# Kernel tuning notes

Hardware: AMD Instinct MI355X
Metric: run time of the kernel (lower is better)

## Reference

```python
import jax, jax.numpy as jnp
import numpy as np

WINDOW_SIZE = 100  # band half-width = WINDOW_SIZE // 2 = 50, inclusive


def setup_inputs() -> dict:
    key = jax.random.key(0)
    kq, kk, kv = jax.random.split(key, 3)
    shape = (2, 8, 4096, 64)  # [B, H, S, D]
    return {
        "query": jax.random.normal(kq, shape, dtype=jnp.float32),
        "key": jax.random.normal(kk, shape, dtype=jnp.float32),
        "value": jax.random.normal(kv, shape, dtype=jnp.float32),
    }


def reference(query, key, value):
    B, H, S, D = query.shape
    half = WINDOW_SIZE // 2
    scale = 1.0 / jnp.sqrt(jnp.asarray(D, dtype=jnp.float32))
    # Full dense scores (faithful to the original module): [B, H, S, S]
    scores = jnp.einsum("bhqd,bhkd->bhqk", query, key) * scale
    # Sliding-window band mask: row i attends to j in [i-half, i+half]
    idx = jnp.arange(S)
    band = jnp.abs(idx[:, None] - idx[None, :]) <= half  # [S, S]
    scores = jnp.where(band[None, None, :, :], scores, -jnp.inf)
    attn = jax.nn.softmax(scores, axis=-1)
    attn = jnp.nan_to_num(attn, nan=0.0)  # matches torch.nan_to_num(w, 0.0)
    return jnp.einsum("bhqk,bhkd->bhqd", attn, value)
```

## Files before the change

### kernel.cpp

```cpp
#include <hip/hip_runtime.h>

#define S_LEN 4096
#define DIM   64
#define HALF  50
#define RB    128
#define WQ    16
#define THREADS 512
#define KCAP  256
#define SCALE 0.125f

typedef __attribute__((ext_vector_type(8))) short bf16x8;
typedef __attribute__((ext_vector_type(4))) float f32x4;

__device__ __forceinline__ unsigned int bf16_rne(float f) {
    unsigned int u = __float_as_uint(f);
    return (u + 0x7fffu + ((u >> 16) & 1u)) >> 16;
}
__device__ __forceinline__ unsigned int pk2(float lo, float hi) {
    return bf16_rne(lo) | (bf16_rne(hi) << 16);
}

__global__ __launch_bounds__(THREADS)
void lattn_mfma(const float* __restrict__ Q, const float* __restrict__ K,
                const float* __restrict__ V, float* __restrict__ O) {
    __shared__ unsigned short Ks[KCAP * 64];
    __shared__ unsigned short Vs[DIM * KCAP];
    __shared__ unsigned short Ps[8 * 16 * 40];

    const int nwg = gridDim.x;
    const int cpx = nwg >> 3;
    const int bid = blockIdx.x;
    const int logical = (bid & 7) * cpx + (bid >> 3);
    const int bh = logical >> 5;
    const int r0 = (logical & 31) * RB;

    const size_t base = (size_t)bh * (S_LEN * DIM);
    const float* Qg = Q + base;
    const float* Kg = K + base;
    const float* Vg = V + base;
    float*       Og = O + base;

    const int kstart = (r0 >= HALF) ? ((r0 - HALF) & ~31) : 0;
    const int kend   = min(S_LEN, r0 + RB + HALF);
    const int nstep  = (kend - kstart + 31) >> 5;
    const int nkeys  = nstep << 5;

    const int u = threadIdx.x;

    for (int idx = u; idx < (nkeys << 3); idx += THREADS) {
        const int krow = idx >> 3;
        const int oct  = idx & 7;
        const int kg   = kstart + krow;
        unsigned int w0, w1, w2, w3;
        if (kg < kend) {
            const float4 a = *(const float4*)(Kg + (size_t)kg * DIM + oct * 8);
            const float4 b = *(const float4*)(Kg + (size_t)kg * DIM + oct * 8 + 4);
            w0 = pk2(a.x, a.y); w1 = pk2(a.z, a.w);
            w2 = pk2(b.x, b.y); w3 = pk2(b.z, b.w);
        } else { w0 = w1 = w2 = w3 = 0u; }
        *(uint4*)(Ks + krow * 64 + ((oct ^ (krow & 7)) << 3)) = make_uint4(w0, w1, w2, w3);
    }

    for (int idx = u; idx < (nkeys << 2); idx += THREADS) {
        const int kp = idx >> 3;
        const int m  = idx & 7;
        const int d0 = m * 8;
        const int k0 = kp * 2;
        const int kg = kstart + k0;
        unsigned int pw[8];
        if (kg < kend) {
            const float* va = Vg + (size_t)kg * DIM + d0;
            const float* vb = va + DIM;
            float a0[8], a1[8];
            *(float4*)a0 = *(const float4*)va;  *(float4*)(a0 + 4) = *(const float4*)(va + 4);
            *(float4*)a1 = *(const float4*)vb;  *(float4*)(a1 + 4) = *(const float4*)(vb + 4);
            #pragma unroll
            for (int j = 0; j < 8; ++j) pw[j] = pk2(a0[j], a1[j]);
        } else {
            #pragma unroll
            for (int j = 0; j < 8; ++j) pw[j] = 0u;
        }
        #pragma unroll
        for (int j = 0; j < 8; ++j) {
            const int jj = (j + m) & 7;
            const int d  = d0 + jj;
            const int sl = (k0 >> 3) ^ (d & 7);
            *(unsigned int*)(Vs + d * KCAP + sl * 8 + (k0 & 7)) = pw[jj];
        }
    }

    const int lane = u & 63;
    const int wv_  = u >> 6;
    const int g  = lane >> 4;
    const int cc = lane & 15;
    const int qlo = r0 + WQ * wv_;

    bf16x8 qf[2];
    #pragma unroll
    for (int ds = 0; ds < 2; ++ds) {
        const float* src = Qg + (size_t)(qlo + cc) * DIM + ds * 32 + g * 8;
        const float4 a = *(const float4*)src;
        const float4 b = *(const float4*)(src + 4);
        uint4 t = make_uint4(pk2(a.x * SCALE, a.y * SCALE), pk2(a.z * SCALE, a.w * SCALE),
                             pk2(b.x * SCALE, b.y * SCALE), pk2(b.z * SCALE, b.w * SCALE));
        qf[ds] = __builtin_bit_cast(bf16x8, t);
    }

    __syncthreads();

    f32x4 oacc[4] = {};
    float denom = 0.f;

    int lo = (qlo >= HALF) ? (qlo - HALF) : 0;
    lo = max(kstart, lo & ~31);
    const int t0 = (lo - kstart) >> 5;
    const int hi = min(kend, qlo + WQ - 1 + HALF + 1);
    const int t1 = (hi - kstart + 31) >> 5;

    unsigned short* Pw = Ps + wv_ * (16 * 40);

    for (int st = t0; st < t1; ++st) {
        const int kb = st << 5;

        f32x4 sacc[2] = {};
        #pragma unroll
        for (int ds = 0; ds < 2; ++ds) {
            #pragma unroll
            for (int kt = 0; kt < 2; ++kt) {
                const int krow = kb + kt * 16 + cc;
                const int sl   = (ds * 4 + g) ^ (krow & 7);
                const bf16x8 ka = *(const bf16x8*)(Ks + krow * 64 + sl * 8);
                sacc[kt] = __builtin_amdgcn_mfma_f32_16x16x32_bf16(ka, qf[ds], sacc[kt], 0, 0, 0);
            }
        }

        const int q = qlo + cc;
        #pragma unroll
        for (int kt = 0; kt < 2; ++kt) {
            float w4[4];
            const int keyb = kstart + kb + kt * 16 + g * 4;
            #pragma unroll
            for (int r = 0; r < 4; ++r) {
                const int key = keyb + r;
                const float e = __expf(sacc[kt][r]);
                const int dd  = key - q;
                const bool ok = (dd >= -HALF) && (dd <= HALF) && (key < S_LEN);
                w4[r] = ok ? e : 0.f;
                denom += w4[r];
            }
            *(uint2*)(Pw + cc * 40 + kt * 16 + g * 4) = make_uint2(pk2(w4[0], w4[1]), pk2(w4[2], w4[3]));
        }

        const bf16x8 pf = *(const bf16x8*)(Pw + cc * 40 + g * 8);
        #pragma unroll
        for (int dt = 0; dt < 4; ++dt) {
            const int d  = dt * 16 + cc;
            const int sl = ((kb >> 3) + g) ^ (d & 7);
            const bf16x8 vf = *(const bf16x8*)(Vs + d * KCAP + sl * 8);
            oacc[dt] = __builtin_amdgcn_mfma_f32_16x16x32_bf16(vf, pf, oacc[dt], 0, 0, 0);
        }
    }

    denom += __shfl_xor(denom, 16);
    denom += __shfl_xor(denom, 32);
    const float rinv = 1.f / denom;
    float* dst = Og + (size_t)(qlo + cc) * DIM;
    #pragma unroll
    for (int dt = 0; dt < 4; ++dt) {
        const f32x4 o = oacc[dt];
        *(float4*)(dst + dt * 16 + g * 4) =
            make_float4(o[0] * rinv, o[1] * rinv, o[2] * rinv, o[3] * rinv);
    }
}

extern "C" void kernel_launch(void* const* d_in, const int* in_sizes, int n_in,
                              void* d_out, int out_size, void* d_ws, size_t ws_size,
                              hipStream_t stream) {
    const float* q = (const float*)d_in[0];
    const float* k = (const float*)d_in[1];
    const float* v = (const float*)d_in[2];
    float* o = (float*)d_out;
    const int nbh = in_sizes[0] / (S_LEN * DIM);
    dim3 grid((S_LEN / RB) * nbh);
    lattn_mfma<<<grid, THREADS, 0, stream>>>(q, k, v, o);
}
```

Before: 22.45 us.

## Process two row blocks per workgroup with register-staged double-buffered K/V loads

Each workgroup now handles two consecutive 128-row blocks. The second block's K/V global loads are issued into registers before the first block's attention compute, then written to a second LDS buffer afterwards, so memory latency overlaps with MFMA work. The grid is halved, which cuts parallelism to 256 workgroups and doubles LDS use per workgroup, and that may lower occupancy. It also adds a clamp on the exponent input and an extra XOR term in the V swizzle.

```diff
diff --git a/kernel.cpp b/kernel.cpp
--- a/kernel.cpp
+++ b/kernel.cpp
@@ -19,95 +19,16 @@
 __device__ __forceinline__ unsigned int pk2(float lo, float hi) {
     return bf16_rne(lo) | (bf16_rne(hi) << 16);
 }
-
-__global__ __launch_bounds__(THREADS)
-void lattn_mfma(const float* __restrict__ Q, const float* __restrict__ K,
-                const float* __restrict__ V, float* __restrict__ O) {
-    __shared__ unsigned short Ks[KCAP * 64];
-    __shared__ unsigned short Vs[DIM * KCAP];
-    __shared__ unsigned short Ps[8 * 16 * 40];
-
-    const int nwg = gridDim.x;
-    const int cpx = nwg >> 3;
-    const int bid = blockIdx.x;
-    const int logical = (bid & 7) * cpx + (bid >> 3);
-    const int bh = logical >> 5;
-    const int r0 = (logical & 31) * RB;
-
-    const size_t base = (size_t)bh * (S_LEN * DIM);
-    const float* Qg = Q + base;
-    const float* Kg = K + base;
-    const float* Vg = V + base;
-    float*       Og = O + base;
-
-    const int kstart = (r0 >= HALF) ? ((r0 - HALF) & ~31) : 0;
-    const int kend   = min(S_LEN, r0 + RB + HALF);
-    const int nstep  = (kend - kstart + 31) >> 5;
-    const int nkeys  = nstep << 5;
-
-    const int u = threadIdx.x;
-
-    for (int idx = u; idx < (nkeys << 3); idx += THREADS) {
-        const int krow = idx >> 3;
-        const int oct  = idx & 7;
-        const int kg   = kstart + krow;
-        unsigned int w0, w1, w2, w3;
-        if (kg < kend) {
-            const float4 a = *(const float4*)(Kg + (size_t)kg * DIM + oct * 8);
-            const float4 b = *(const float4*)(Kg + (size_t)kg * DIM + oct * 8 + 4);
-            w0 = pk2(a.x, a.y); w1 = pk2(a.z, a.w);
-            w2 = pk2(b.x, b.y); w3 = pk2(b.z, b.w);
-        } else { w0 = w1 = w2 = w3 = 0u; }
-        *(uint4*)(Ks + krow * 64 + ((oct ^ (krow & 7)) << 3)) = make_uint4(w0, w1, w2, w3);
-    }
-
-    for (int idx = u; idx < (nkeys << 2); idx += THREADS) {
-        const int kp = idx >> 3;
-        const int m  = idx & 7;
-        const int d0 = m * 8;
-        const int k0 = kp * 2;
-        const int kg = kstart + k0;
-        unsigned int pw[8];
-        if (kg < kend) {
-            const float* va = Vg + (size_t)kg * DIM + d0;
-            const float* vb = va + DIM;
-            float a0[8], a1[8];
-            *(float4*)a0 = *(const float4*)va;  *(float4*)(a0 + 4) = *(const float4*)(va + 4);
-            *(float4*)a1 = *(const float4*)vb;  *(float4*)(a1 + 4) = *(const float4*)(vb + 4);
-            #pragma unroll
-            for (int j = 0; j < 8; ++j) pw[j] = pk2(a0[j], a1[j]);
-        } else {
-            #pragma unroll
-            for (int j = 0; j < 8; ++j) pw[j] = 0u;
-        }
-        #pragma unroll
-        for (int j = 0; j < 8; ++j) {
-            const int jj = (j + m) & 7;
-            const int d  = d0 + jj;
-            const int sl = (k0 >> 3) ^ (d & 7);
-            *(unsigned int*)(Vs + d * KCAP + sl * 8 + (k0 & 7)) = pw[jj];
-        }
-    }
-
-    const int lane = u & 63;
-    const int wv_  = u >> 6;
-    const int g  = lane >> 4;
-    const int cc = lane & 15;
-    const int qlo = r0 + WQ * wv_;
-
-    bf16x8 qf[2];
-    #pragma unroll
-    for (int ds = 0; ds < 2; ++ds) {
-        const float* src = Qg + (size_t)(qlo + cc) * DIM + ds * 32 + g * 8;
-        const float4 a = *(const float4*)src;
-        const float4 b = *(const float4*)(src + 4);
-        uint4 t = make_uint4(pk2(a.x * SCALE, a.y * SCALE), pk2(a.z * SCALE, a.w * SCALE),
-                             pk2(b.x * SCALE, b.y * SCALE), pk2(b.z * SCALE, b.w * SCALE));
-        qf[ds] = __builtin_bit_cast(bf16x8, t);
-    }
-
-    __syncthreads();
-
+__device__ __forceinline__ bf16x8 cvt8(float4 a, float4 b) {
+    uint4 t = make_uint4(pk2(a.x, a.y), pk2(a.z, a.w), pk2(b.x, b.y), pk2(b.z, b.w));
+    return __builtin_bit_cast(bf16x8, t);
+}
+
+__device__ __forceinline__ void attend_store(
+    const unsigned short* __restrict__ Ksb, const unsigned short* __restrict__ Vsb,
+    unsigned short* __restrict__ Pw, const bf16x8* qf,
+    int kstart, int kend, int qlo, int g, int cc, float* __restrict__ Og)
+{
     f32x4 oacc[4] = {};
     float denom = 0.f;
 
@@ -117,20 +38,18 @@
     const int hi = min(kend, qlo + WQ - 1 + HALF + 1);
     const int t1 = (hi - kstart + 31) >> 5;
 
-    unsigned short* Pw = Ps + wv_ * (16 * 40);
-
     for (int st = t0; st < t1; ++st) {
-        const int kb = st << 5;
+        const int kb32 = st << 5;
 
         f32x4 sacc[2] = {};
         #pragma unroll
         for (int ds = 0; ds < 2; ++ds) {
             #pragma unroll
             for (int kt = 0; kt < 2; ++kt) {
-                const int krow = kb + kt * 16 + cc;
+                const int krow = kb32 + kt * 16 + cc;
                 const int sl   = (ds * 4 + g) ^ (krow & 7);
-                const bf16x8 ka = *(const bf16x8*)(Ks + krow * 64 + sl * 8);
-                sacc[kt] = __builtin_amdgcn_mfma_f32_16x16x32_bf16(ka, qf[ds], sacc[kt], 0, 0, 0);
+                const bf16x8 kfr = *(const bf16x8*)(Ksb + krow * 64 + sl * 8);
+                sacc[kt] = __builtin_amdgcn_mfma_f32_16x16x32_bf16(kfr, qf[ds], sacc[kt], 0, 0, 0);
             }
         }
 
@@ -138,25 +57,26 @@
         #pragma unroll
         for (int kt = 0; kt < 2; ++kt) {
             float w4[4];
-            const int keyb = kstart + kb + kt * 16 + g * 4;
+            const int keyb = kstart + kb32 + kt * 16 + g * 4;
             #pragma unroll
             for (int r = 0; r < 4; ++r) {
                 const int key = keyb + r;
-                const float e = __expf(sacc[kt][r]);
+                const float e = __expf(fminf(sacc[kt][r], 60.f));
                 const int dd  = key - q;
                 const bool ok = (dd >= -HALF) && (dd <= HALF) && (key < S_LEN);
                 w4[r] = ok ? e : 0.f;
                 denom += w4[r];
             }
-            *(uint2*)(Pw + cc * 40 + kt * 16 + g * 4) = make_uint2(pk2(w4[0], w4[1]), pk2(w4[2], w4[3]));
-        }
-
+            *(uint2*)(Pw + cc * 40 + kt * 16 + g * 4) =
+                make_uint2(pk2(w4[0], w4[1]), pk2(w4[2], w4[3]));
+        }
         const bf16x8 pf = *(const bf16x8*)(Pw + cc * 40 + g * 8);
+
         #pragma unroll
         for (int dt = 0; dt < 4; ++dt) {
             const int d  = dt * 16 + cc;
-            const int sl = ((kb >> 3) + g) ^ (d & 7);
-            const bf16x8 vf = *(const bf16x8*)(Vs + d * KCAP + sl * 8);
+            const int sl = ((kb32 >> 3) + g) ^ (d & 7) ^ ((d >> 3) & 7);
+            const bf16x8 vf = *(const bf16x8*)(Vsb + d * KCAP + sl * 8);
             oacc[dt] = __builtin_amdgcn_mfma_f32_16x16x32_bf16(vf, pf, oacc[dt], 0, 0, 0);
         }
     }
@@ -173,6 +93,127 @@
     }
 }
 
+__global__ __launch_bounds__(THREADS)
+void lattn_mfma(const float* __restrict__ Q, const float* __restrict__ K,
+                const float* __restrict__ V, float* __restrict__ O) {
+    __shared__ unsigned short Ks[2][KCAP * 64];
+    __shared__ unsigned short Vs[2][DIM * KCAP];
+    __shared__ unsigned short Ps[8 * 16 * 40];
+
+    const int nwg = gridDim.x;
+    const int cpx = nwg >> 3;
+    const int bid = blockIdx.x;
+    const int logical = (bid & 7) * cpx + (bid >> 3);
+    const int bh = logical >> 4;
+    const int R0 = (logical & 15) * (2 * RB);
+
+    const size_t base = (size_t)bh * (S_LEN * DIM);
+    const float* Qg = Q + base;
+    const float* Kg = K + base;
+    const float* Vg = V + base;
+    float*       Og = O + base;
+
+    const int u = threadIdx.x;
+    const int lane = u & 63;
+    const int wv_  = u >> 6;
+    const int g  = lane >> 4;
+    const int cc = lane & 15;
+
+    const int r0a = R0, r0b = R0 + RB;
+    const int ksa = (r0a >= HALF) ? ((r0a - HALF) & ~31) : 0;
+    const int kea = min(S_LEN, r0a + RB + HALF);
+    const int ksb = (r0b - HALF) & ~31;
+    const int keb = min(S_LEN, r0b + RB + HALF);
+    const int qloa = r0a + WQ * wv_;
+    const int qlob = r0b + WQ * wv_;
+
+    bf16x8 qfa[2], qfb[2];
+    #pragma unroll
+    for (int ds = 0; ds < 2; ++ds) {
+        const float* sa = Qg + (size_t)(qloa + cc) * DIM + ds * 32 + g * 8;
+        const float* sb = Qg + (size_t)(qlob + cc) * DIM + ds * 32 + g * 8;
+        float4 a = *(const float4*)sa, b = *(const float4*)(sa + 4);
+        float4 c = *(const float4*)sb, d = *(const float4*)(sb + 4);
+        a.x*=SCALE;a.y*=SCALE;a.z*=SCALE;a.w*=SCALE; b.x*=SCALE;b.y*=SCALE;b.z*=SCALE;b.w*=SCALE;
+        c.x*=SCALE;c.y*=SCALE;c.z*=SCALE;c.w*=SCALE; d.x*=SCALE;d.y*=SCALE;d.z*=SCALE;d.w*=SCALE;
+        qfa[ds] = cvt8(a, b);
+        qfb[ds] = cvt8(c, d);
+    }
+
+    float4 kr[4][2], vr[2][4];
+
+    auto k_load = [&](int kstart, int kend) {
+        #pragma unroll
+        for (int i = 0; i < 4; ++i) {
+            const int idx = u + i * THREADS;
+            const int kg  = kstart + (idx >> 3);
+            const int oct = idx & 7;
+            if (kg < kend) {
+                const float* p = Kg + (size_t)kg * DIM + oct * 8;
+                kr[i][0] = *(const float4*)p; kr[i][1] = *(const float4*)(p + 4);
+            } else {
+                kr[i][0] = make_float4(0.f,0.f,0.f,0.f); kr[i][1] = kr[i][0];
+            }
+        }
+    };
+    auto k_write = [&](unsigned short* Kb) {
+        #pragma unroll
+        for (int i = 0; i < 4; ++i) {
+            const int idx  = u + i * THREADS;
+            const int krow = idx >> 3;
+            const int oct  = idx & 7;
+            *(uint4*)(Kb + krow * 64 + ((oct ^ (krow & 7)) << 3)) =
+                __builtin_bit_cast(uint4, cvt8(kr[i][0], kr[i][1]));
+        }
+    };
+    auto v_load = [&](int kstart, int kend) {
+        #pragma unroll
+        for (int i = 0; i < 2; ++i) {
+            const int idx = u + i * THREADS;
+            const int kg  = kstart + (idx >> 3) * 2;
+            const int d0  = (idx & 7) * 8;
+            if (kg < kend) {
+                const float* p = Vg + (size_t)kg * DIM + d0;
+                vr[i][0] = *(const float4*)p;         vr[i][1] = *(const float4*)(p + 4);
+                vr[i][2] = *(const float4*)(p + DIM); vr[i][3] = *(const float4*)(p + DIM + 4);
+            } else {
+                vr[i][0] = make_float4(0.f,0.f,0.f,0.f);
+                vr[i][1] = vr[i][0]; vr[i][2] = vr[i][0]; vr[i][3] = vr[i][0];
+            }
+        }
+    };
+    auto v_write = [&](unsigned short* Vb) {
+        #pragma unroll
+        for (int i = 0; i < 2; ++i) {
+            const int idx = u + i * THREADS;
+            const int k0  = (idx >> 3) * 2;
+            const int m   = idx & 7;
+            const float* a0 = (const float*)&vr[i][0];
+            const float* a1 = (const float*)&vr[i][2];
+            #pragma unroll
+            for (int j = 0; j < 8; ++j) {
+                const int d  = m * 8 + j;
+                const int sl = (k0 >> 3) ^ j ^ m;
+                *(unsigned int*)(Vb + d * KCAP + sl * 8 + (k0 & 7)) = pk2(a0[j], a1[j]);
+            }
+        }
+    };
+
+    k_load(ksa, kea); v_load(ksa, kea);
+    k_write(Ks[0]);   v_write(Vs[0]);
+    __syncthreads();
+
+    k_load(ksb, keb); v_load(ksb, keb);
+    __builtin_amdgcn_sched_barrier(0);
+
+    unsigned short* Pw = Ps + wv_ * (16 * 40);
+    attend_store(Ks[0], Vs[0], Pw, qfa, ksa, kea, qloa, g, cc, Og);
+
+    k_write(Ks[1]); v_write(Vs[1]);
+    __syncthreads();
+    attend_store(Ks[1], Vs[1], Pw, qfb, ksb, keb, qlob, g, cc, Og);
+}
+
 extern "C" void kernel_launch(void* const* d_in, const int* in_sizes, int n_in,
                               void* d_out, int out_size, void* d_ws, size_t ws_size,
                               hipStream_t stream) {
@@ -181,6 +222,6 @@
     const float* v = (const float*)d_in[2];
     float* o = (float*)d_out;
     const int nbh = in_sizes[0] / (S_LEN * DIM);
-    dim3 grid((S_LEN / RB) * nbh);
+    dim3 grid((S_LEN / (2 * RB)) * nbh);
     lattn_mfma<<<grid, THREADS, 0, stream>>>(q, k, v, o);
 }
```

Result: slower. 42.73 us (+90.4%).
